# Kernel tuning notes

Hardware: AMD Instinct MI355X
Metric: run time of the kernel (lower is better)

Reference implementation:

```python
import jax, jax.numpy as jnp
import numpy as np

EPS_BN = 1e-5

def _bn(x, gamma, beta):
    # BatchNorm1d with track_running_stats=False: batch stats over all rows
    H = x.shape[-1]
    x2 = x.reshape(-1, H)
    mu = x2.mean(axis=0)
    var = x2.var(axis=0)  # biased, as torch BN uses for normalization
    y = gamma * (x2 - mu) / jnp.sqrt(var + EPS_BN) + beta
    return y.reshape(x.shape)


def setup_inputs() -> dict:
    key = jax.random.key(0)
    ks = jax.random.split(key, 9)
    B, Vsc, Vst, H = 2, 256, 256, 256
    return {
        'h_sc': jax.random.normal(ks[0], (B, Vsc, H), jnp.float32),
        'h_st': jax.random.normal(ks[1], (B, Vst, H), jnp.float32),
        'bi_e': jax.random.normal(ks[2], (B, Vsc, Vst, H), jnp.float32),
        'bi_graph': jax.random.uniform(ks[3], (B, Vsc, Vst), jnp.float32),
        'sc_e': jax.random.normal(ks[4], (B, Vsc, Vsc, H), jnp.float32),
        'sc_graph': jax.random.uniform(ks[5], (B, Vsc, Vsc), jnp.float32),
        'st_e': jax.random.normal(ks[6], (B, Vst, Vst, H), jnp.float32),
        'st_graph': jax.random.uniform(ks[7], (B, Vst, Vst), jnp.float32),
        'Ws': jax.random.normal(ks[8], (15, H, H), jnp.float32) / jnp.sqrt(jnp.float32(H)),
        'bs': jnp.zeros((15, H), jnp.float32),
        'gamma_h': jnp.ones((H,), jnp.float32),
        'beta_h': jnp.zeros((H,), jnp.float32),
        'gamma_e': jnp.ones((H,), jnp.float32),
        'beta_e': jnp.zeros((H,), jnp.float32),
    }

# Linear slot order: 0 U1, 1 U2, 2 V1, 3 V2, 4 W1, 5 W2,
#                    6 bi_A, 7 bi_B, 8 bi_C, 9 sc_A, 10 sc_B, 11 sc_C,
#                    12 st_A, 13 st_B, 14 st_C

def reference(h_sc, h_st, bi_e, bi_graph, sc_e, sc_graph, st_e, st_graph,
              Ws, bs, gamma_h, beta_h, gamma_e, beta_e):
    lin = lambda x, i: jnp.einsum('...h,oh->...o', x, Ws[i]) + bs[i]

    h_sc_in, h_st_in = h_sc, h_st
    bi_e_in, sc_e_in, st_e_in = bi_e, sc_e, st_e

    Uh_sc, Uh_st = lin(h_sc, 0), lin(h_st, 1)
    Vh_sc, Vh_st = lin(h_sc, 2), lin(h_st, 3)
    Wh_sc, Wh_st = lin(h_sc, 4), lin(h_st, 5)

    # e_ij = A h_i + B h_j + C e_ij  (broadcast over the V x V grid)
    bi_e2 = lin(h_sc, 6)[:, :, None, :] + lin(h_st, 7)[:, None, :, :] + lin(bi_e, 8)
    sc_e2 = lin(h_sc, 9)[:, :, None, :] + lin(h_sc, 10)[:, None, :, :] + lin(sc_e, 11)
    st_e2 = lin(h_st, 12)[:, :, None, :] + lin(h_st, 13)[:, None, :, :] + lin(st_e, 14)

    bi_g = jax.nn.sigmoid(bi_e2)
    sc_g = jax.nn.sigmoid(sc_e2)
    st_g = jax.nn.sigmoid(st_e2)

    # sum aggregation: h_i += sum_j gate_ij * Vh_j (over the neighbor axis)
    h_sc2 = Uh_sc \
        + jnp.einsum('bijh,bjh->bih', bi_g, Vh_st) \
        + jnp.einsum('bijh,bjh->bih', sc_g, Wh_sc)
    h_st2 = Uh_st \
        + jnp.einsum('bijh,bih->bjh', bi_g, Vh_sc) \
        + jnp.einsum('bijh,bih->bjh', st_g, Wh_st)

    h_sc2 = _bn(h_sc2, gamma_h, beta_h)
    h_st2 = _bn(h_st2, gamma_h, beta_h)
    bi_e2 = _bn(bi_e2, gamma_e, beta_e)
    sc_e2 = _bn(sc_e2, gamma_e, beta_e)
    st_e2 = _bn(st_e2, gamma_e, beta_e)

    # relu + residual (mode='residual')
    h_sc_out = h_sc_in + jax.nn.relu(h_sc2)
    h_st_out = h_st_in + jax.nn.relu(h_st2)
    bi_e_out = bi_e_in + jax.nn.relu(bi_e2)
    sc_e_out = sc_e_in + jax.nn.relu(sc_e2)
    st_e_out = st_e_in + jax.nn.relu(st_e2)
    return (h_sc_out, h_st_out, bi_e_out, sc_e_out, st_e_out)
```

## Files before the change

### kernel.cpp

```cpp
#include <hip/hip_runtime.h>

typedef unsigned short ushort_t;
using floatx4 = __attribute__((ext_vector_type(4))) float;
using shortx8 = __attribute__((ext_vector_type(8))) short;

#define NROWS_E 131072
#define E_ELEMS 33554432
#define H_ROWS  512
#define H_ELEMS 131072

__device__ __forceinline__ ushort_t f2bf(float f) {
    union { float f; unsigned int u; } x; x.f = f;
    unsigned int r = (x.u + 0x7FFFu + ((x.u >> 16) & 1u)) >> 16;
    return (ushort_t)r;
}

__global__ void k_convW(const float* __restrict__ Ws, ushort_t* __restrict__ Wb) {
    int idx = blockIdx.x * 256 + threadIdx.x;
    int t = idx >> 16;
    int r = idx & 65535;
    int slot = (t == 0) ? 8 : (t == 1) ? 11 : 14;
    Wb[idx] = f2bf(Ws[slot * 65536 + r]);
}

__launch_bounds__(256)
__global__ void k_lin(const float* __restrict__ hsc, const float* __restrict__ hst,
                      const float* __restrict__ Ws, const float* __restrict__ bs,
                      float* __restrict__ tH) {
    int bx = blockIdx.x;
    int s = bx >> 5; int rem = bx & 31; int mt = rem >> 2; int nt = rem & 3;
    const int wsl[12] = {0,1,2,3,4,5,6,7,9,10,12,13};
    const int xst[12] = {0,1,0,1,0,1,0,1,0,0,1,1};
    int wslot = wsl[s];
    const float* x = xst[s] ? hst : hsc;
    int m0 = mt * 64, n0 = nt * 64;
    __shared__ float Xs[64][33];
    __shared__ float Wt[64][33];
    int tid = threadIdx.x;
    int tn = tid & 15, tm = tid >> 4;
    float acc[4][4] = {};
    for (int kk = 0; kk < 8; ++kk) {
        int k0 = kk * 32;
        #pragma unroll
        for (int u = tid; u < 2048; u += 256) {
            int r = u >> 5, k = u & 31;
            Xs[r][k] = x[(m0 + r) * 256 + k0 + k];
            Wt[r][k] = Ws[wslot * 65536 + (n0 + r) * 256 + k0 + k];
        }
        __syncthreads();
        #pragma unroll
        for (int k = 0; k < 32; ++k) {
            float a[4], b[4];
            #pragma unroll
            for (int i = 0; i < 4; ++i) a[i] = Xs[tm*4+i][k];
            #pragma unroll
            for (int j = 0; j < 4; ++j) b[j] = Wt[tn*4+j][k];
            #pragma unroll
            for (int i = 0; i < 4; ++i)
                #pragma unroll
                for (int j = 0; j < 4; ++j) acc[i][j] += a[i]*b[j];
        }
        __syncthreads();
    }
    #pragma unroll
    for (int i = 0; i < 4; ++i)
        #pragma unroll
        for (int j = 0; j < 4; ++j) {
            int n = n0 + tn*4 + j;
            tH[(long)s * H_ELEMS + (long)(m0 + tm*4 + i) * 256 + n] = acc[i][j] + bs[wslot*256 + n];
        }
}

__launch_bounds__(256, 3)
__global__ void k_passb(const float* __restrict__ e_bi, const float* __restrict__ e_sc,
                        const float* __restrict__ e_st,
                        const float* __restrict__ tH, const ushort_t* __restrict__ Wb,
                        const float* __restrict__ bs,
                        float* __restrict__ outE,
                        float* __restrict__ accSc, float* __restrict__ accSt,
                        float* __restrict__ S1, float* __restrict__ S2) {
    int bx = blockIdx.x;
    int t = bx >> 11;
    int rem = bx & 2047;
    int b = rem >> 10;
    int rem2 = rem & 1023;
    int i0 = (rem2 >> 5) * 8;
    int j0 = (rem2 & 31) * 8;

    const float *e, *tA, *tB, *wj, *wi;
    int doSj, doSi, slotC;
    if (t == 0)      { e = e_bi; tA = tH + 6L*H_ELEMS; tB = tH + 7L*H_ELEMS; wj = tH + 3L*H_ELEMS; wi = tH + 2L*H_ELEMS; doSj = 1; doSi = 1; slotC = 8; }
    else if (t == 1) { e = e_sc; tA = tH + 8L*H_ELEMS; tB = tH + 9L*H_ELEMS; wj = tH + 4L*H_ELEMS; wi = tH;             doSj = 1; doSi = 0; slotC = 11; }
    else             { e = e_st; tA = tH + 10L*H_ELEMS; tB = tH + 11L*H_ELEMS; wj = tH;            wi = tH + 5L*H_ELEMS; doSj = 0; doSi = 1; slotC = 14; }

    __shared__ ushort_t As[64 * 32];
    __shared__ ushort_t Bs[256 * 32];
    __shared__ float tAs[8 * 256];
    __shared__ float tBs[8 * 256];
    __shared__ float wjs[8 * 256];
    __shared__ float wis[8 * 256];

    int tid = threadIdx.x;
    #pragma unroll
    for (int u = tid; u < 2048; u += 256) {
        int r = u >> 8, c = u & 255;
        tAs[u] = tA[(long)(b*256 + i0 + r) * 256 + c];
        tBs[u] = tB[(long)(b*256 + j0 + r) * 256 + c] + bs[slotC*256 + c];
        wjs[u] = wj[(long)(b*256 + j0 + r) * 256 + c];
        wis[u] = wi[(long)(b*256 + i0 + r) * 256 + c];
    }

    const ushort_t* WbT = Wb + (long)t * 65536;
    int lane = tid & 63;
    int wave_n = tid >> 6;
    int fc = lane & 15;
    int quad = lane >> 4;

    floatx4 acc[4][4];
    #pragma unroll
    for (int i = 0; i < 4; ++i)
        #pragma unroll
        for (int j = 0; j < 4; ++j) acc[i][j] = (floatx4){0.f, 0.f, 0.f, 0.f};

    int slr = tid >> 2;
    int skq = (tid & 3) * 8;
    int siloc = slr >> 3, sjloc = slr & 7;
    const float* arow = e + ((long)(b*256 + i0 + siloc) * 256 + (j0 + sjloc)) * 256;

    for (int kk = 0; kk < 8; ++kk) {
        int k0 = kk * 32;
        float4 f0 = *(const float4*)(arow + k0 + skq);
        float4 f1 = *(const float4*)(arow + k0 + skq + 4);
        shortx8 pk;
        pk[0] = (short)f2bf(f0.x); pk[1] = (short)f2bf(f0.y);
        pk[2] = (short)f2bf(f0.z); pk[3] = (short)f2bf(f0.w);
        pk[4] = (short)f2bf(f1.x); pk[5] = (short)f2bf(f1.y);
        pk[6] = (short)f2bf(f1.z); pk[7] = (short)f2bf(f1.w);
        *(shortx8*)&As[slr*32 + skq] = pk;
        const uint4* bsrc = (const uint4*)(WbT + (long)tid * 256 + k0);
        uint4* bdst = (uint4*)&Bs[tid * 32];
        #pragma unroll
        for (int q = 0; q < 4; ++q) bdst[q] = bsrc[q];
        __syncthreads();
        shortx8 af[4];
        #pragma unroll
        for (int mt = 0; mt < 4; ++mt)
            af[mt] = *(const shortx8*)&As[(mt*16 + fc)*32 + quad*8];
        #pragma unroll
        for (int nt = 0; nt < 4; ++nt) {
            shortx8 bf = *(const shortx8*)&Bs[(wave_n*64 + nt*16 + fc)*32 + quad*8];
            #pragma unroll
            for (int mt = 0; mt < 4; ++mt)
                acc[mt][nt] = __builtin_amdgcn_mfma_f32_16x16x32_bf16(af[mt], bf, acc[mt][nt], 0, 0, 0);
        }
        __syncthreads();
    }

    float s1[4] = {0,0,0,0}, s2[4] = {0,0,0,0};
    float sst[4][4] = {};
    long outBase = (long)t * E_ELEMS;
    #pragma unroll
    for (int nt = 0; nt < 4; ++nt) {
        int cloc = wave_n*64 + nt*16 + fc;
        #pragma unroll
        for (int mt = 0; mt < 4; ++mt) {
            int iloc = 2*mt + (quad >> 1);
            float tAv = tAs[iloc*256 + cloc];
            float wiv = wis[iloc*256 + cloc];
            float p = 0.f;
            #pragma unroll
            for (int r = 0; r < 4; ++r) {
                int jloc = (quad & 1)*4 + r;
                float v = acc[mt][nt][r] + tAv + tBs[jloc*256 + cloc];
                s1[nt] += v; s2[nt] += v*v;
                float g = 1.f / (1.f + __expf(-v));
                long grow = (long)(b*256 + i0 + iloc) * 256 + (j0 + jloc);
                outE[outBase + grow*256 + cloc] = v;
                if (doSj) p += g * wjs[jloc*256 + cloc];
                if (doSi) sst[nt][r] += g * wiv;
            }
            if (doSj) {
                p += __shfl_xor(p, 16);
                if ((quad & 1) == 0)
                    atomicAdd(&accSc[(long)(b*256 + i0 + iloc)*256 + cloc], p);
            }
        }
        if (doSi) {
            #pragma unroll
            for (int r = 0; r < 4; ++r) {
                float vv = sst[nt][r] + __shfl_xor(sst[nt][r], 32);
                if (quad < 2) {
                    int jloc = (quad & 1)*4 + r;
                    atomicAdd(&accSt[(long)(b*256 + j0 + jloc)*256 + cloc], vv);
                }
            }
        }
        float a1 = s1[nt]; a1 += __shfl_xor(a1, 16); a1 += __shfl_xor(a1, 32);
        float a2 = s2[nt]; a2 += __shfl_xor(a2, 16); a2 += __shfl_xor(a2, 32);
        if (quad == 0) {
            atomicAdd(&S1[t*256 + cloc], a1);
            atomicAdd(&S2[t*256 + cloc], a2);
        }
    }
}

__global__ void k_bnp(const float* __restrict__ S1, const float* __restrict__ S2,
                      const float* __restrict__ ge, const float* __restrict__ be,
                      float* __restrict__ scale, float* __restrict__ shift) {
    int t = blockIdx.x, c = threadIdx.x;
    float N = (float)NROWS_E;
    float mean = S1[t*256 + c] / N;
    float var = S2[t*256 + c] / N - mean*mean;
    float rs = rsqrtf(var + 1e-5f);
    float sc = ge[c] * rs;
    scale[t*256 + c] = sc;
    shift[t*256 + c] = be[c] - sc * mean;
}

__global__ void k_hfin(const float* __restrict__ tH, const float* __restrict__ accSc,
                       const float* __restrict__ accSt,
                       const float* __restrict__ hsc, const float* __restrict__ hst,
                       const float* __restrict__ gh, const float* __restrict__ bh,
                       float* __restrict__ outp) {
    int tau = blockIdx.x >> 8;
    int c = blockIdx.x & 255;
    const float* U = tH + (tau ? (long)H_ELEMS : 0L);
    const float* A = tau ? accSt : accSc;
    const float* hin = tau ? hst : hsc;
    int lane = threadIdx.x;
    float v[8]; float s1 = 0.f, s2 = 0.f;
    #pragma unroll
    for (int k = 0; k < 8; ++k) {
        int row = lane + k*64;
        float x = U[(long)row*256 + c] + A[(long)row*256 + c];
        v[k] = x; s1 += x; s2 += x*x;
    }
    #pragma unroll
    for (int off = 1; off < 64; off <<= 1) { s1 += __shfl_xor(s1, off); s2 += __shfl_xor(s2, off); }
    float mean = s1 / 512.f;
    float var = s2 / 512.f - mean*mean;
    float rs = rsqrtf(var + 1e-5f);
    float gc = gh[c], bc = bh[c];
    #pragma unroll
    for (int k = 0; k < 8; ++k) {
        int row = lane + k*64;
        float y = gc * (v[k] - mean) * rs + bc;
        outp[(long)tau*H_ELEMS + (long)row*256 + c] = hin[(long)row*256 + c] + fmaxf(y, 0.f);
    }
}

__launch_bounds__(256)
__global__ void k_efin(const float* __restrict__ e_bi, const float* __restrict__ e_sc,
                       const float* __restrict__ e_st,
                       const float* __restrict__ scale, const float* __restrict__ shift,
                       float* __restrict__ outE) {
    long idx4 = (long)blockIdx.x * 256 + threadIdx.x;
    long fi = idx4 * 4;
    int t = (int)(fi >> 25);
    long within = fi & (long)(E_ELEMS - 1);
    int c = (int)(fi & 255);
    const float* ein = (t == 0) ? e_bi : (t == 1) ? e_sc : e_st;
    float4 sc4 = *(const float4*)&scale[t*256 + c];
    float4 sh4 = *(const float4*)&shift[t*256 + c];
    float4 v = *(const float4*)&outE[fi];
    float4 e4 = *(const float4*)&ein[within];
    float4 r;
    r.x = e4.x + fmaxf(sc4.x*v.x + sh4.x, 0.f);
    r.y = e4.y + fmaxf(sc4.y*v.y + sh4.y, 0.f);
    r.z = e4.z + fmaxf(sc4.z*v.z + sh4.z, 0.f);
    r.w = e4.w + fmaxf(sc4.w*v.w + sh4.w, 0.f);
    *(float4*)&outE[fi] = r;
}

extern "C" void kernel_launch(void* const* d_in, const int* in_sizes, int n_in,
                              void* d_out, int out_size, void* d_ws, size_t ws_size,
                              hipStream_t stream) {
    (void)in_sizes; (void)n_in; (void)out_size; (void)ws_size;
    const float* h_sc = (const float*)d_in[0];
    const float* h_st = (const float*)d_in[1];
    const float* bi_e = (const float*)d_in[2];
    const float* sc_e = (const float*)d_in[4];
    const float* st_e = (const float*)d_in[6];
    const float* Ws   = (const float*)d_in[8];
    const float* bs   = (const float*)d_in[9];
    const float* gh   = (const float*)d_in[10];
    const float* bh   = (const float*)d_in[11];
    const float* ge   = (const float*)d_in[12];
    const float* be   = (const float*)d_in[13];
    float* out = (float*)d_out;

    float* ws = (float*)d_ws;
    float* tH      = ws;
    float* accSc   = ws + 1572864;
    float* accSt   = ws + 1703936;
    float* S1      = ws + 1835008;
    float* S2      = ws + 1835776;
    float* bnScale = ws + 1836544;
    float* bnShift = ws + 1837312;
    ushort_t* Wb   = (ushort_t*)(ws + 1838080);

    hipMemsetAsync(accSc, 0, (size_t)(131072*2 + 1536) * sizeof(float), stream);
    k_convW<<<768, 256, 0, stream>>>(Ws, Wb);
    k_lin<<<384, 256, 0, stream>>>(h_sc, h_st, Ws, bs, tH);
    k_passb<<<6144, 256, 0, stream>>>(bi_e, sc_e, st_e, tH, Wb, bs,
                                      out + 262144, accSc, accSt, S1, S2);
    k_bnp<<<3, 256, 0, stream>>>(S1, S2, ge, be, bnScale, bnShift);
    k_hfin<<<512, 64, 0, stream>>>(tH, accSc, accSt, h_sc, h_st, gh, bh, out);
    k_efin<<<98304, 256, 0, stream>>>(bi_e, sc_e, st_e, bnScale, bnShift, out + 262144);
}
```

Before: 1.155 ms.

## Recompute the edge GEMM in a second pass instead of storing the pre-BN edges

The edge kernel is split into two passes. The first pass computes the GEMM only to accumulate the gated aggregations and the BN sums, and no longer writes pre-BN edge values. A second pass recomputes the GEMM and applies BN, ReLU and the residual directly, which replaces the separate elementwise finalize kernel and its full read and write of the intermediate edge tensor. Both passes drop LDS staging and load A/B fragments straight from global memory into registers with one-step software prefetch. The cost is doubling the MFMA work and a second read of the edge inputs, with less coalesced fragment loads.

```diff
diff --git a/kernel.cpp b/kernel.cpp
--- a/kernel.cpp
+++ b/kernel.cpp
@@ -71,12 +71,11 @@
         }
 }
 
-__launch_bounds__(256, 3)
-__global__ void k_passb(const float* __restrict__ e_bi, const float* __restrict__ e_sc,
+__launch_bounds__(256)
+__global__ void k_pass1(const float* __restrict__ e_bi, const float* __restrict__ e_sc,
                         const float* __restrict__ e_st,
                         const float* __restrict__ tH, const ushort_t* __restrict__ Wb,
                         const float* __restrict__ bs,
-                        float* __restrict__ outE,
                         float* __restrict__ accSc, float* __restrict__ accSt,
                         float* __restrict__ S1, float* __restrict__ S2) {
     int bx = blockIdx.x;
@@ -93,96 +92,111 @@
     else if (t == 1) { e = e_sc; tA = tH + 8L*H_ELEMS; tB = tH + 9L*H_ELEMS; wj = tH + 4L*H_ELEMS; wi = tH;             doSj = 1; doSi = 0; slotC = 11; }
     else             { e = e_st; tA = tH + 10L*H_ELEMS; tB = tH + 11L*H_ELEMS; wj = tH;            wi = tH + 5L*H_ELEMS; doSj = 0; doSi = 1; slotC = 14; }
 
-    __shared__ ushort_t As[64 * 32];
-    __shared__ ushort_t Bs[256 * 32];
-    __shared__ float tAs[8 * 256];
-    __shared__ float tBs[8 * 256];
-    __shared__ float wjs[8 * 256];
-    __shared__ float wis[8 * 256];
-
+    const ushort_t* WbT = Wb + (long)t * 65536;
     int tid = threadIdx.x;
-    #pragma unroll
-    for (int u = tid; u < 2048; u += 256) {
-        int r = u >> 8, c = u & 255;
-        tAs[u] = tA[(long)(b*256 + i0 + r) * 256 + c];
-        tBs[u] = tB[(long)(b*256 + j0 + r) * 256 + c] + bs[slotC*256 + c];
-        wjs[u] = wj[(long)(b*256 + j0 + r) * 256 + c];
-        wis[u] = wi[(long)(b*256 + i0 + r) * 256 + c];
-    }
-
-    const ushort_t* WbT = Wb + (long)t * 65536;
     int lane = tid & 63;
     int wave_n = tid >> 6;
     int fc = lane & 15;
     int quad = lane >> 4;
 
+    long abase[4];
+    #pragma unroll
+    for (int mt = 0; mt < 4; ++mt) {
+        int mloc = mt*16 + fc;
+        abase[mt] = ((long)(b*256 + i0 + (mloc >> 3)) * 256 + (j0 + (mloc & 7))) * 256 + quad*8;
+    }
+    long bbase = (long)(wave_n*64 + fc) * 256 + quad*8;
+
     floatx4 acc[4][4];
     #pragma unroll
     for (int i = 0; i < 4; ++i)
         #pragma unroll
         for (int j = 0; j < 4; ++j) acc[i][j] = (floatx4){0.f, 0.f, 0.f, 0.f};
 
-    int slr = tid >> 2;
-    int skq = (tid & 3) * 8;
-    int siloc = slr >> 3, sjloc = slr & 7;
-    const float* arow = e + ((long)(b*256 + i0 + siloc) * 256 + (j0 + sjloc)) * 256;
-
+    float4 a0[4], a1[4];
+    shortx8 bfv[4];
+    #pragma unroll
+    for (int mt = 0; mt < 4; ++mt) {
+        a0[mt] = *(const float4*)(e + abase[mt]);
+        a1[mt] = *(const float4*)(e + abase[mt] + 4);
+    }
+    #pragma unroll
+    for (int nt = 0; nt < 4; ++nt)
+        bfv[nt] = *(const shortx8*)(WbT + bbase + nt*4096);
+
+    #pragma unroll 2
     for (int kk = 0; kk < 8; ++kk) {
-        int k0 = kk * 32;
-        float4 f0 = *(const float4*)(arow + k0 + skq);
-        float4 f1 = *(const float4*)(arow + k0 + skq + 4);
-        shortx8 pk;
-        pk[0] = (short)f2bf(f0.x); pk[1] = (short)f2bf(f0.y);
-        pk[2] = (short)f2bf(f0.z); pk[3] = (short)f2bf(f0.w);
-        pk[4] = (short)f2bf(f1.x); pk[5] = (short)f2bf(f1.y);
-        pk[6] = (short)f2bf(f1.z); pk[7] = (short)f2bf(f1.w);
-        *(shortx8*)&As[slr*32 + skq] = pk;
-        const uint4* bsrc = (const uint4*)(WbT + (long)tid * 256 + k0);
-        uint4* bdst = (uint4*)&Bs[tid * 32];
-        #pragma unroll
-        for (int q = 0; q < 4; ++q) bdst[q] = bsrc[q];
-        __syncthreads();
+        float4 c0[4], c1[4]; shortx8 cb[4];
+        if (kk < 7) {
+            int k0 = (kk + 1) * 32;
+            #pragma unroll
+            for (int mt = 0; mt < 4; ++mt) {
+                c0[mt] = *(const float4*)(e + abase[mt] + k0);
+                c1[mt] = *(const float4*)(e + abase[mt] + k0 + 4);
+            }
+            #pragma unroll
+            for (int nt = 0; nt < 4; ++nt)
+                cb[nt] = *(const shortx8*)(WbT + bbase + nt*4096 + k0);
+        }
         shortx8 af[4];
         #pragma unroll
-        for (int mt = 0; mt < 4; ++mt)
-            af[mt] = *(const shortx8*)&As[(mt*16 + fc)*32 + quad*8];
-        #pragma unroll
-        for (int nt = 0; nt < 4; ++nt) {
-            shortx8 bf = *(const shortx8*)&Bs[(wave_n*64 + nt*16 + fc)*32 + quad*8];
+        for (int mt = 0; mt < 4; ++mt) {
+            shortx8 pk;
+            pk[0] = (short)f2bf(a0[mt].x); pk[1] = (short)f2bf(a0[mt].y);
+            pk[2] = (short)f2bf(a0[mt].z); pk[3] = (short)f2bf(a0[mt].w);
+            pk[4] = (short)f2bf(a1[mt].x); pk[5] = (short)f2bf(a1[mt].y);
+            pk[6] = (short)f2bf(a1[mt].z); pk[7] = (short)f2bf(a1[mt].w);
+            af[mt] = pk;
+        }
+        #pragma unroll
+        for (int nt = 0; nt < 4; ++nt)
             #pragma unroll
             for (int mt = 0; mt < 4; ++mt)
-                acc[mt][nt] = __builtin_amdgcn_mfma_f32_16x16x32_bf16(af[mt], bf, acc[mt][nt], 0, 0, 0);
-        }
-        __syncthreads();
-    }
-
-    float s1[4] = {0,0,0,0}, s2[4] = {0,0,0,0};
+                acc[mt][nt] = __builtin_amdgcn_mfma_f32_16x16x32_bf16(af[mt], bfv[nt], acc[mt][nt], 0, 0, 0);
+        if (kk < 7) {
+            #pragma unroll
+            for (int mt = 0; mt < 4; ++mt) { a0[mt] = c0[mt]; a1[mt] = c1[mt]; }
+            #pragma unroll
+            for (int nt = 0; nt < 4; ++nt) bfv[nt] = cb[nt];
+        }
+    }
+
+    float s1[4], s2[4];
+    #pragma unroll
+    for (int nt = 0; nt < 4; ++nt) { s1[nt] = 0.f; s2[nt] = 0.f; }
     float sst[4][4] = {};
-    long outBase = (long)t * E_ELEMS;
+
     #pragma unroll
     for (int nt = 0; nt < 4; ++nt) {
         int cloc = wave_n*64 + nt*16 + fc;
+        float bias_c = bs[slotC*256 + cloc];
+        float tBv[4], wjv[4];
+        #pragma unroll
+        for (int r = 0; r < 4; ++r) {
+            int jloc = (quad & 1)*4 + r;
+            long jidx = (long)(b*256 + j0 + jloc)*256 + cloc;
+            tBv[r] = tB[jidx] + bias_c;
+            wjv[r] = doSj ? wj[jidx] : 0.f;
+        }
         #pragma unroll
         for (int mt = 0; mt < 4; ++mt) {
             int iloc = 2*mt + (quad >> 1);
-            float tAv = tAs[iloc*256 + cloc];
-            float wiv = wis[iloc*256 + cloc];
+            long iidx = (long)(b*256 + i0 + iloc)*256 + cloc;
+            float tAv = tA[iidx];
+            float wiv = doSi ? wi[iidx] : 0.f;
             float p = 0.f;
             #pragma unroll
             for (int r = 0; r < 4; ++r) {
-                int jloc = (quad & 1)*4 + r;
-                float v = acc[mt][nt][r] + tAv + tBs[jloc*256 + cloc];
+                float v = acc[mt][nt][r] + tAv + tBv[r];
                 s1[nt] += v; s2[nt] += v*v;
                 float g = 1.f / (1.f + __expf(-v));
-                long grow = (long)(b*256 + i0 + iloc) * 256 + (j0 + jloc);
-                outE[outBase + grow*256 + cloc] = v;
-                if (doSj) p += g * wjs[jloc*256 + cloc];
+                if (doSj) p += g * wjv[r];
                 if (doSi) sst[nt][r] += g * wiv;
             }
             if (doSj) {
                 p += __shfl_xor(p, 16);
                 if ((quad & 1) == 0)
-                    atomicAdd(&accSc[(long)(b*256 + i0 + iloc)*256 + cloc], p);
+                    atomicAdd(&accSc[iidx], p);
             }
         }
         if (doSi) {
@@ -195,11 +209,11 @@
                 }
             }
         }
-        float a1 = s1[nt]; a1 += __shfl_xor(a1, 16); a1 += __shfl_xor(a1, 32);
-        float a2 = s2[nt]; a2 += __shfl_xor(a2, 16); a2 += __shfl_xor(a2, 32);
+        float a1s = s1[nt]; a1s += __shfl_xor(a1s, 16); a1s += __shfl_xor(a1s, 32);
+        float a2s = s2[nt]; a2s += __shfl_xor(a2s, 16); a2s += __shfl_xor(a2s, 32);
         if (quad == 0) {
-            atomicAdd(&S1[t*256 + cloc], a1);
-            atomicAdd(&S2[t*256 + cloc], a2);
+            atomicAdd(&S1[t*256 + cloc], a1s);
+            atomicAdd(&S2[t*256 + cloc], a2s);
         }
     }
 }
@@ -250,26 +264,121 @@
 }
 
 __launch_bounds__(256)
-__global__ void k_efin(const float* __restrict__ e_bi, const float* __restrict__ e_sc,
-                       const float* __restrict__ e_st,
-                       const float* __restrict__ scale, const float* __restrict__ shift,
-                       float* __restrict__ outE) {
-    long idx4 = (long)blockIdx.x * 256 + threadIdx.x;
-    long fi = idx4 * 4;
-    int t = (int)(fi >> 25);
-    long within = fi & (long)(E_ELEMS - 1);
-    int c = (int)(fi & 255);
-    const float* ein = (t == 0) ? e_bi : (t == 1) ? e_sc : e_st;
-    float4 sc4 = *(const float4*)&scale[t*256 + c];
-    float4 sh4 = *(const float4*)&shift[t*256 + c];
-    float4 v = *(const float4*)&outE[fi];
-    float4 e4 = *(const float4*)&ein[within];
-    float4 r;
-    r.x = e4.x + fmaxf(sc4.x*v.x + sh4.x, 0.f);
-    r.y = e4.y + fmaxf(sc4.y*v.y + sh4.y, 0.f);
-    r.z = e4.z + fmaxf(sc4.z*v.z + sh4.z, 0.f);
-    r.w = e4.w + fmaxf(sc4.w*v.w + sh4.w, 0.f);
-    *(float4*)&outE[fi] = r;
+__global__ void k_pass2(const float* __restrict__ e_bi, const float* __restrict__ e_sc,
+                        const float* __restrict__ e_st,
+                        const float* __restrict__ tH, const ushort_t* __restrict__ Wb,
+                        const float* __restrict__ bs,
+                        const float* __restrict__ bnScale, const float* __restrict__ bnShift,
+                        float* __restrict__ outE) {
+    int bx = blockIdx.x;
+    int t = bx >> 11;
+    int rem = bx & 2047;
+    int b = rem >> 10;
+    int rem2 = rem & 1023;
+    int i0 = (rem2 >> 5) * 8;
+    int j0 = (rem2 & 31) * 8;
+
+    const float *e, *tA, *tB;
+    int slotC;
+    if (t == 0)      { e = e_bi; tA = tH + 6L*H_ELEMS; tB = tH + 7L*H_ELEMS; slotC = 8; }
+    else if (t == 1) { e = e_sc; tA = tH + 8L*H_ELEMS; tB = tH + 9L*H_ELEMS; slotC = 11; }
+    else             { e = e_st; tA = tH + 10L*H_ELEMS; tB = tH + 11L*H_ELEMS; slotC = 14; }
+
+    const ushort_t* WbT = Wb + (long)t * 65536;
+    int tid = threadIdx.x;
+    int lane = tid & 63;
+    int wave_n = tid >> 6;
+    int fc = lane & 15;
+    int quad = lane >> 4;
+
+    long abase[4];
+    #pragma unroll
+    for (int mt = 0; mt < 4; ++mt) {
+        int mloc = mt*16 + fc;
+        abase[mt] = ((long)(b*256 + i0 + (mloc >> 3)) * 256 + (j0 + (mloc & 7))) * 256 + quad*8;
+    }
+    long bbase = (long)(wave_n*64 + fc) * 256 + quad*8;
+
+    floatx4 acc[4][4];
+    #pragma unroll
+    for (int i = 0; i < 4; ++i)
+        #pragma unroll
+        for (int j = 0; j < 4; ++j) acc[i][j] = (floatx4){0.f, 0.f, 0.f, 0.f};
+
+    float4 a0[4], a1[4];
+    shortx8 bfv[4];
+    #pragma unroll
+    for (int mt = 0; mt < 4; ++mt) {
+        a0[mt] = *(const float4*)(e + abase[mt]);
+        a1[mt] = *(const float4*)(e + abase[mt] + 4);
+    }
+    #pragma unroll
+    for (int nt = 0; nt < 4; ++nt)
+        bfv[nt] = *(const shortx8*)(WbT + bbase + nt*4096);
+
+    #pragma unroll 2
+    for (int kk = 0; kk < 8; ++kk) {
+        float4 c0[4], c1[4]; shortx8 cb[4];
+        if (kk < 7) {
+            int k0 = (kk + 1) * 32;
+            #pragma unroll
+            for (int mt = 0; mt < 4; ++mt) {
+                c0[mt] = *(const float4*)(e + abase[mt] + k0);
+                c1[mt] = *(const float4*)(e + abase[mt] + k0 + 4);
+            }
+            #pragma unroll
+            for (int nt = 0; nt < 4; ++nt)
+                cb[nt] = *(const shortx8*)(WbT + bbase + nt*4096 + k0);
+        }
+        shortx8 af[4];
+        #pragma unroll
+        for (int mt = 0; mt < 4; ++mt) {
+            shortx8 pk;
+            pk[0] = (short)f2bf(a0[mt].x); pk[1] = (short)f2bf(a0[mt].y);
+            pk[2] = (short)f2bf(a0[mt].z); pk[3] = (short)f2bf(a0[mt].w);
+            pk[4] = (short)f2bf(a1[mt].x); pk[5] = (short)f2bf(a1[mt].y);
+            pk[6] = (short)f2bf(a1[mt].z); pk[7] = (short)f2bf(a1[mt].w);
+            af[mt] = pk;
+        }
+        #pragma unroll
+        for (int nt = 0; nt < 4; ++nt)
+            #pragma unroll
+            for (int mt = 0; mt < 4; ++mt)
+                acc[mt][nt] = __builtin_amdgcn_mfma_f32_16x16x32_bf16(af[mt], bfv[nt], acc[mt][nt], 0, 0, 0);
+        if (kk < 7) {
+            #pragma unroll
+            for (int mt = 0; mt < 4; ++mt) { a0[mt] = c0[mt]; a1[mt] = c1[mt]; }
+            #pragma unroll
+            for (int nt = 0; nt < 4; ++nt) bfv[nt] = cb[nt];
+        }
+    }
+
+    long outBase = (long)t * E_ELEMS;
+    #pragma unroll
+    for (int nt = 0; nt < 4; ++nt) {
+        int cloc = wave_n*64 + nt*16 + fc;
+        float bias_c = bs[slotC*256 + cloc];
+        float sc = bnScale[t*256 + cloc];
+        float sh = bnShift[t*256 + cloc];
+        float tBv[4];
+        #pragma unroll
+        for (int r = 0; r < 4; ++r) {
+            int jloc = (quad & 1)*4 + r;
+            tBv[r] = tB[(long)(b*256 + j0 + jloc)*256 + cloc] + bias_c;
+        }
+        #pragma unroll
+        for (int mt = 0; mt < 4; ++mt) {
+            int iloc = 2*mt + (quad >> 1);
+            float tAv = tA[(long)(b*256 + i0 + iloc)*256 + cloc];
+            #pragma unroll
+            for (int r = 0; r < 4; ++r) {
+                int jloc = (quad & 1)*4 + r;
+                float v = acc[mt][nt][r] + tAv + tBv[r];
+                long grow = ((long)(b*256 + i0 + iloc)*256 + (j0 + jloc))*256 + cloc;
+                outE[outBase + grow] = e[grow] + fmaxf(sc*v + sh, 0.f);
+            }
+        }
+    }
 }
 
 extern "C" void kernel_launch(void* const* d_in, const int* in_sizes, int n_in,
@@ -302,9 +411,10 @@
     hipMemsetAsync(accSc, 0, (size_t)(131072*2 + 1536) * sizeof(float), stream);
     k_convW<<<768, 256, 0, stream>>>(Ws, Wb);
     k_lin<<<384, 256, 0, stream>>>(h_sc, h_st, Ws, bs, tH);
-    k_passb<<<6144, 256, 0, stream>>>(bi_e, sc_e, st_e, tH, Wb, bs,
-                                      out + 262144, accSc, accSt, S1, S2);
+    k_pass1<<<6144, 256, 0, stream>>>(bi_e, sc_e, st_e, tH, Wb, bs,
+                                      accSc, accSt, S1, S2);
     k_bnp<<<3, 256, 0, stream>>>(S1, S2, ge, be, bnScale, bnShift);
     k_hfin<<<512, 64, 0, stream>>>(tH, accSc, accSt, h_sc, h_st, gh, bh, out);
-    k_efin<<<98304, 256, 0, stream>>>(bi_e, sc_e, st_e, bnScale, bnShift, out + 262144);
-}
+    k_pass2<<<6144, 256, 0, stream>>>(bi_e, sc_e, st_e, tH, Wb, bs,
+                                      bnScale, bnShift, out + 262144);
+}
```

Result: slower. 1.272 ms (+10.1%).
